# Kernel tuning notes

Measured on AMD Instinct MI355X. Metric: run time of the kernel, lower is better.

Reference implementation:

```python
import jax, jax.numpy as jnp
import numpy as np

B, H, W, C = 32, 56, 56, 384
HEADS, WIN, SHIFT = 12, 7, 3
MLP_HID = 4 * C
N = WIN * WIN
EPS = 1e-5


def _rel_pos_index(win):
    ch, cw = np.meshgrid(np.arange(win), np.arange(win), indexing='ij')
    coords = np.stack([ch.ravel(), cw.ravel()])            # (2, N)
    rel = coords[:, :, None] - coords[:, None, :]          # (2, N, N)
    rel = rel.transpose(1, 2, 0).astype(np.int64)
    rel[:, :, 0] += win - 1
    rel[:, :, 1] += win - 1
    rel[:, :, 0] *= 2 * win - 1
    return rel.sum(-1)                                     # (N, N)


def _attn_mask(Hh, Ww, win, shift):
    img = np.zeros((Hh, Ww))
    cnt = 0
    slices = (slice(0, -win), slice(-win, -shift), slice(-shift, None))
    for hs in slices:
        for ws in slices:
            img[hs, ws] = cnt
            cnt += 1
    m = img.reshape(Hh // win, win, Ww // win, win).transpose(0, 2, 1, 3).reshape(-1, win * win)
    am = m[:, None, :] - m[:, :, None]
    return np.where(am != 0, -100.0, 0.0).astype(np.float32)  # (nW, N, N)


REL_IDX = jnp.asarray(_rel_pos_index(WIN))
ATTN_MASK = jnp.asarray(_attn_mask(H, W, WIN, SHIFT))


def setup_inputs() -> dict:
    key = jax.random.key(0)
    ks = jax.random.split(key, 16)
    s = 0.02
    return {
        'x': jax.random.normal(ks[0], (B, H * W, C), jnp.float32),
        'g1': jnp.ones((C,), jnp.float32),
        'b1': jnp.zeros((C,), jnp.float32),
        'qkv_w': jax.random.normal(ks[1], (3 * C, C), jnp.float32) * s,
        'qkv_b': jnp.zeros((3 * C,), jnp.float32),
        'rel_bias': jax.random.normal(ks[2], ((2 * WIN - 1) ** 2, HEADS), jnp.float32) * s,
        'proj_w': jax.random.normal(ks[3], (C, C), jnp.float32) * s,
        'proj_b': jnp.zeros((C,), jnp.float32),
        'g2': jnp.ones((C,), jnp.float32),
        'b2': jnp.zeros((C,), jnp.float32),
        'fc1_w': jax.random.normal(ks[4], (MLP_HID, C), jnp.float32) * s,
        'fc1_b': jnp.zeros((MLP_HID,), jnp.float32),
        'fc2_w': jax.random.normal(ks[5], (C, MLP_HID), jnp.float32) * s,
        'fc2_b': jnp.zeros((C,), jnp.float32),
    }


def _ln(x, g, b):
    m = x.mean(-1, keepdims=True)
    v = jnp.var(x, axis=-1, keepdims=True)
    return (x - m) * jax.lax.rsqrt(v + EPS) * g + b


def reference(x, g1, b1, qkv_w, qkv_b, rel_bias, proj_w, proj_b, g2, b2, fc1_w, fc1_b, fc2_w, fc2_b):
    Bz, L, Cc = x.shape
    hd = Cc // HEADS
    nWh = H // WIN
    shortcut = x

    h = _ln(x, g1, b1).reshape(Bz, H, W, Cc)
    h = jnp.roll(h, (-SHIFT, -SHIFT), axis=(1, 2))
    # window partition -> (Bz*nW, N, C)
    h = h.reshape(Bz, nWh, WIN, nWh, WIN, Cc).transpose(0, 1, 3, 2, 4, 5).reshape(-1, N, Cc)

    qkv = (h @ qkv_w.T + qkv_b).reshape(-1, N, 3, HEADS, hd).transpose(2, 0, 3, 1, 4)
    q, k, v = qkv[0] * (hd ** -0.5), qkv[1], qkv[2]
    attn = jnp.einsum('bhnd,bhmd->bhnm', q, k)  # (Bz*nW, heads, N, N)

    bias = rel_bias[REL_IDX.reshape(-1)].reshape(N, N, HEADS).transpose(2, 0, 1)
    attn = attn + bias[None]

    nW = ATTN_MASK.shape[0]
    attn = attn.reshape(Bz, nW, HEADS, N, N) + ATTN_MASK[None, :, None]
    attn = jax.nn.softmax(attn, axis=-1).reshape(-1, HEADS, N, N)

    out = jnp.einsum('bhnm,bhmd->bhnd', attn, v).transpose(0, 2, 1, 3).reshape(-1, N, Cc)
    out = out @ proj_w.T + proj_b
    # window reverse + unshift
    out = out.reshape(Bz, nWh, nWh, WIN, WIN, Cc).transpose(0, 1, 3, 2, 4, 5).reshape(Bz, H, W, Cc)
    out = jnp.roll(out, (SHIFT, SHIFT), axis=(1, 2)).reshape(Bz, L, Cc)

    x = shortcut + out
    h2 = _ln(x, g2, b2)
    h2 = jax.nn.gelu(h2 @ fc1_w.T + fc1_b, approximate=False)
    h2 = h2 @ fc2_w.T + fc2_b
    return x + h2
```

## Files before the change

kernel.cpp:

```cpp
#include <hip/hip_runtime.h>
#include <hip/hip_bf16.h>
#include <math.h>

#define B_      32
#define H_      56
#define W_      56
#define C_      384
#define HEADS_  12
#define WIN_    7
#define SHIFT_  3
#define NTOK_   49
#define HD_     32
#define T_      100352
#define MLP_    1536
#define TCH_    50176

typedef __bf16 bf16x8 __attribute__((ext_vector_type(8)));
typedef unsigned short u16x8 __attribute__((ext_vector_type(8)));
typedef float  f32x4  __attribute__((ext_vector_type(4)));

__device__ __forceinline__ float bf2f(unsigned short u) {
  union { unsigned int i; float f; } v; v.i = ((unsigned int)u) << 16; return v.f;
}
__device__ __forceinline__ unsigned short f2bf(float f) {
  union { float f; unsigned int i; } v; v.f = f;
  unsigned int x = v.i;
  return (unsigned short)((x + 0x7fffu + ((x >> 16) & 1u)) >> 16);
}
__device__ __forceinline__ float gelu_fast(float x) {
  const float t = 0.79788456f * x * (1.0f + 0.044715f * x * x);
  const float e = __expf(2.0f * t);
  const float th = 1.0f - 2.0f / (e + 1.0f);
  return 0.5f * x * (1.0f + th);
}
__device__ __forceinline__ void gload_lds16(const void* g, void* l) {
  __builtin_amdgcn_global_load_lds(
      (const __attribute__((address_space(1))) void*)g,
      (__attribute__((address_space(3))) void*)l, 16, 0, 0);
}
__device__ __forceinline__ bf16x8 ldg8(const unsigned short* p) {
  u16x8 v = *(const u16x8*)p;
  return __builtin_bit_cast(bf16x8, v);
}

__global__ __launch_bounds__(256)
void wconv_all_kernel(const float* __restrict__ s0, unsigned short* __restrict__ d0,
                      const float* __restrict__ s1, unsigned short* __restrict__ d1,
                      const float* __restrict__ s2, unsigned short* __restrict__ d2,
                      const float* __restrict__ s3, unsigned short* __restrict__ d3) {
  int b = blockIdx.x;
  const float* src; unsigned short* dst;
  if (b < 432)       { src = s0; dst = d0; }
  else if (b < 576)  { src = s1; dst = d1; b -= 432; }
  else if (b < 1152) { src = s2; dst = d2; b -= 576; }
  else               { src = s3; dst = d3; b -= 1152; }
  const int i = (b * 256 + threadIdx.x) * 4;
  const float4 v = *(const float4*)(src + i);
  ushort4 o;
  o.x = f2bf(v.x); o.y = f2bf(v.y); o.z = f2bf(v.z); o.w = f2bf(v.w);
  *(ushort4*)(dst + i) = o;
}

template<int REMAP>
__global__ __launch_bounds__(256)
void ln_kernel(const float* __restrict__ xin, const float* __restrict__ g,
               const float* __restrict__ bb, unsigned short* __restrict__ outbf) {
  const int m = blockIdx.x * 4 + (threadIdx.x >> 6);
  const int lane = threadIdx.x & 63;
  size_t src;
  if (REMAP) {
    int w = m / NTOK_, t = m - w * NTOK_;
    int bz = w >> 6, widx = w & 63;
    int wh = widx >> 3, ww = widx & 7;
    int ih = t / WIN_, iw = t - ih * WIN_;
    int gh = (wh * WIN_ + ih + SHIFT_) % H_;
    int gw = (ww * WIN_ + iw + SHIFT_) % W_;
    src = ((size_t)bz * (H_ * W_) + gh * W_ + gw) * C_;
  } else {
    src = (size_t)m * C_;
  }
  const float* row = xin + src;
  float v[6]; float s = 0.f, s2 = 0.f;
#pragma unroll
  for (int u = 0; u < 6; ++u) {
    v[u] = row[lane + 64 * u];
    s += v[u]; s2 += v[u] * v[u];
  }
#pragma unroll
  for (int off = 32; off; off >>= 1) {
    s  += __shfl_xor(s, off);
    s2 += __shfl_xor(s2, off);
  }
  const float mean = s * (1.0f / C_);
  const float var  = s2 * (1.0f / C_) - mean * mean;
  const float rstd = rsqrtf(var + 1e-5f);
  unsigned short* orow = outbf + (size_t)m * C_;
#pragma unroll
  for (int u = 0; u < 6; ++u) {
    int c = lane + 64 * u;
    orow[c] = f2bf((v[u] - mean) * rstd * g[c] + bb[c]);
  }
}

#define BM 256
#define BN 128
#define BKg 64

template<int EPI>
__global__ __launch_bounds__(512)
void mfma_gemm(const unsigned short* __restrict__ A,
               const unsigned short* __restrict__ Wb,
               const float* __restrict__ bias,
               void* __restrict__ outv,
               const float* __restrict__ resid,
               int M, int Nn, int K) {
  __shared__ unsigned short Al[BM * BKg];
  __shared__ unsigned short Bl[BN * BKg];
  const int t    = threadIdx.x;
  const int wid  = t >> 6;
  const int lane = t & 63;
  const int wr   = wid >> 1, wc = wid & 1;

  const unsigned int nb = gridDim.x * gridDim.y;
  const unsigned int lin = blockIdx.y * gridDim.x + blockIdx.x;
  const unsigned int q = nb >> 3, r = nb & 7;
  const unsigned int xcd = lin & 7, idx = lin >> 3;
  const unsigned int wg = (xcd < r ? xcd * (q + 1) : r * (q + 1) + (xcd - r) * q) + idx;
  const int m0 = (int)(wg / gridDim.x) * BM;
  const int n0 = (int)(wg % gridDim.x) * BN;

  f32x4 acc[4][4] = {};

  const int sr8    = lane >> 3;
  const int schunk = (lane & 7) ^ (sr8 & 7);
  const int fr  = lane & 15;
  const int fq  = lane >> 4;

  for (int k0 = 0; k0 < K; k0 += BKg) {
    __syncthreads();
#pragma unroll
    for (int i = 0; i < 4; ++i) {
      const int rr = i * 64 + wid * 8 + sr8;
      gload_lds16(A + (size_t)(m0 + rr) * K + k0 + schunk * 8,
                  (void*)(Al + (size_t)(i * 64 + wid * 8) * BKg));
    }
#pragma unroll
    for (int i = 0; i < 2; ++i) {
      const int rr = i * 64 + wid * 8 + sr8;
      gload_lds16(Wb + (size_t)(n0 + rr) * K + k0 + schunk * 8,
                  (void*)(Bl + (size_t)(i * 64 + wid * 8) * BKg));
    }
    __syncthreads();

#pragma unroll
    for (int kk = 0; kk < 2; ++kk) {
      bf16x8 af[4], bfr[4];
#pragma unroll
      for (int mi = 0; mi < 4; ++mi) {
        const int row = wr * 64 + mi * 16 + fr;
        const int ch  = (kk * 4 + fq) ^ (row & 7);
        af[mi] = *(const bf16x8*)(Al + (size_t)row * BKg + ch * 8);
      }
#pragma unroll
      for (int ni = 0; ni < 4; ++ni) {
        const int row = wc * 64 + ni * 16 + fr;
        const int ch  = (kk * 4 + fq) ^ (row & 7);
        bfr[ni] = *(const bf16x8*)(Bl + (size_t)row * BKg + ch * 8);
      }
#pragma unroll
      for (int mi = 0; mi < 4; ++mi)
#pragma unroll
        for (int ni = 0; ni < 4; ++ni)
          acc[mi][ni] = __builtin_amdgcn_mfma_f32_16x16x32_bf16(
              af[mi], bfr[ni], acc[mi][ni], 0, 0, 0);
    }
  }

  const int ecol  = fr;
  const int erow0 = fq * 4;
#pragma unroll
  for (int mi = 0; mi < 4; ++mi) {
#pragma unroll
    for (int r2 = 0; r2 < 4; ++r2) {
      const int m = m0 + wr * 64 + mi * 16 + erow0 + r2;
      size_t dstbase = 0;
      if (EPI == 2) {
        int w = m / NTOK_, tt = m - w * NTOK_;
        int bz = w >> 6, widx = w & 63;
        int wh = widx >> 3, ww = widx & 7;
        int ih = tt / WIN_, iw = tt - ih * WIN_;
        int gh = (wh * WIN_ + ih + SHIFT_) % H_;
        int gw = (ww * WIN_ + iw + SHIFT_) % W_;
        dstbase = ((size_t)bz * (H_ * W_) + gh * W_ + gw) * C_;
      }
#pragma unroll
      for (int ni = 0; ni < 4; ++ni) {
        const int n = n0 + wc * 64 + ni * 16 + ecol;
        float val = acc[mi][ni][r2] + bias[n];
        if (EPI == 0) {
          ((unsigned short*)outv)[(size_t)m * Nn + n] = f2bf(val);
        } else if (EPI == 1) {
          ((unsigned short*)outv)[(size_t)m * Nn + n] = f2bf(gelu_fast(val));
        } else if (EPI == 2) {
          ((float*)outv)[dstbase + n] = resid[dstbase + n] + val;
        } else {
          float* o = (float*)outv + (size_t)m * Nn + n;
          *o += val;
        }
      }
    }
  }
}

__global__ __launch_bounds__(64)
void bias_expand_kernel(const float* __restrict__ rel_bias,
                        float* __restrict__ biasx) {
  const int hi = blockIdx.x;
  const int head = hi / NTOK_, i = hi - head * NTOK_;
  const int j = threadIdx.x;
  float v = 0.f;
  if (j < NTOK_) {
    const int ih = i / 7, iw = i - ih * 7;
    const int jh = j / 7, jw = j - jh * 7;
    const int ridx = (ih - jh + 6) * 13 + (iw - jw + 6);
    v = rel_bias[ridx * HEADS_ + head];
  }
  biasx[(size_t)hi * 64 + j] = v;
}

#define AW 2
__global__ __launch_bounds__(64 * AW)
void attn_mfma_kernel(const unsigned short* __restrict__ qkv,
                      const float* __restrict__ biasx,
                      unsigned short* __restrict__ out) {
  __shared__ unsigned short sP[AW][64 * 72];
  __shared__ unsigned short sVT[AW][32 * 72];
  __shared__ float sRI[AW][64];
  const int wid  = threadIdx.x >> 6;
  const int lane = threadIdx.x & 63;
  const int task = blockIdx.x * AW + wid;
  const int w    = task / HEADS_;
  const int head = task - w * HEADS_;
  const int widx = w & 63;
  const int wh = widx >> 3, ww = widx & 7;
  const bool edge = (wh == 7) || (ww == 7);
  const int c  = lane & 15;
  const int fq = lane >> 4;
  unsigned short* Pl = sP[wid];
  unsigned short* Vl = sVT[wid];
  float* Ri = sRI[wid];
  const unsigned short* qw = qkv + (size_t)w * NTOK_ * (3 * C_);

  u16x8 vv[4];
#pragma unroll
  for (int p = 0; p < 4; ++p)
    vv[p] = *(const u16x8*)(qw + (size_t)(p * 16 + c) * (3 * C_) + 2 * C_ + head * HD_ + fq * 8);

  bf16x8 kf[4], qf[4];
#pragma unroll
  for (int nj = 0; nj < 4; ++nj)
    kf[nj] = ldg8(qw + (size_t)(nj * 16 + c) * (3 * C_) + C_ + head * HD_ + fq * 8);
#pragma unroll
  for (int qi = 0; qi < 4; ++qi)
    qf[qi] = ldg8(qw + (size_t)(qi * 16 + c) * (3 * C_) + head * HD_ + fq * 8);

  const f32x4 zero4 = {0.f, 0.f, 0.f, 0.f};
  f32x4 accT[4][4];
#pragma unroll
  for (int nj = 0; nj < 4; ++nj)
#pragma unroll
    for (int qi = 0; qi < 4; ++qi)
      accT[nj][qi] = __builtin_amdgcn_mfma_f32_16x16x32_bf16(kf[nj], qf[qi], zero4, 0, 0, 0);

#pragma unroll
  for (int p = 0; p < 4; ++p)
#pragma unroll
    for (int u = 0; u < 8; ++u)
      Vl[(fq * 8 + u) * 72 + p * 16 + c] = (unsigned short)vv[p][u];

  int lj16[16];
  unsigned jpad = 0;
#pragma unroll
  for (int tt = 0; tt < 16; ++tt) {
    const int j = (tt >> 2) * 16 + fq * 4 + (tt & 3);
    int lj = 0;
    if (j >= NTOK_) jpad |= (1u << tt);
    else if (edge) {
      const int jh = j / 7, jw2 = j - jh * 7;
      const int shj = wh * 7 + jh, swj = ww * 7 + jw2;
      lj = (shj < 49 ? 0 : (shj < 53 ? 1 : 2)) * 3 + (swj < 49 ? 0 : (swj < 53 ? 1 : 2));
    }
    lj16[tt] = lj;
  }

  const float* bh = biasx + (size_t)head * (NTOK_ * 64);
#pragma unroll
  for (int qi = 0; qi < 4; ++qi) {
    const int i  = qi * 16 + c;
    const int ic = i < NTOK_ ? i : 0;
    int li = 0;
    if (edge) {
      const int ih = ic / 7, iw2 = ic - ih * 7;
      const int shi = wh * 7 + ih, swi = ww * 7 + iw2;
      li = (shi < 49 ? 0 : (shi < 53 ? 1 : 2)) * 3 + (swi < 49 ? 0 : (swi < 53 ? 1 : 2));
    }
    float sv[16];
#pragma unroll
    for (int nj = 0; nj < 4; ++nj) {
      const float4 b4 = *(const float4*)(bh + ic * 64 + nj * 16 + fq * 4);
      const float* b4p = (const float*)&b4;
#pragma unroll
      for (int r = 0; r < 4; ++r) {
        const int tt = nj * 4 + r;
        float s = accT[nj][qi][r] * 0.17677669529663687f + b4p[r];
        if (edge && lj16[tt] != li) s -= 100.f;
        if (jpad & (1u << tt)) s = -1e30f;
        sv[tt] = s;
      }
    }
    float mx = sv[0];
#pragma unroll
    for (int tt = 1; tt < 16; ++tt) mx = fmaxf(mx, sv[tt]);
    mx = fmaxf(mx, __shfl_xor(mx, 16));
    mx = fmaxf(mx, __shfl_xor(mx, 32));
    float e[16]; float sm = 0.f;
#pragma unroll
    for (int tt = 0; tt < 16; ++tt) { e[tt] = __expf(sv[tt] - mx); sm += e[tt]; }
    sm += __shfl_xor(sm, 16);
    sm += __shfl_xor(sm, 32);
    if (fq == 0) Ri[i] = 1.0f / sm;
#pragma unroll
    for (int nj = 0; nj < 4; ++nj) {
      ushort4 pk;
      pk.x = f2bf(e[nj * 4 + 0]); pk.y = f2bf(e[nj * 4 + 1]);
      pk.z = f2bf(e[nj * 4 + 2]); pk.w = f2bf(e[nj * 4 + 3]);
      *(ushort4*)(Pl + (size_t)i * 72 + nj * 16 + fq * 4) = pk;
    }
  }

  f32x4 accO[4][2] = {};
#pragma unroll
  for (int kk = 0; kk < 2; ++kk) {
    bf16x8 ap[4], bv[2];
#pragma unroll
    for (int mi = 0; mi < 4; ++mi)
      ap[mi] = __builtin_bit_cast(bf16x8,
          *(const u16x8*)(Pl + (mi * 16 + c) * 72 + kk * 32 + fq * 8));
#pragma unroll
    for (int nd = 0; nd < 2; ++nd)
      bv[nd] = __builtin_bit_cast(bf16x8,
          *(const u16x8*)(Vl + (nd * 16 + c) * 72 + kk * 32 + fq * 8));
#pragma unroll
    for (int mi = 0; mi < 4; ++mi)
#pragma unroll
      for (int nd = 0; nd < 2; ++nd)
        accO[mi][nd] = __builtin_amdgcn_mfma_f32_16x16x32_bf16(ap[mi], bv[nd], accO[mi][nd], 0, 0, 0);
  }

#pragma unroll
  for (int mi = 0; mi < 4; ++mi)
#pragma unroll
    for (int r = 0; r < 4; ++r) {
      const int i = mi * 16 + fq * 4 + r;
      if (i < NTOK_) {
        const float inv = Ri[i];
#pragma unroll
        for (int nd = 0; nd < 2; ++nd)
          out[(size_t)(w * NTOK_ + i) * C_ + head * HD_ + nd * 16 + c] =
              f2bf(accO[mi][nd][r] * inv);
      }
    }
}

extern "C" void kernel_launch(void* const* d_in, const int* in_sizes, int n_in,
                              void* d_out, int out_size, void* d_ws, size_t ws_size,
                              hipStream_t stream) {
  const float* x        = (const float*)d_in[0];
  const float* g1       = (const float*)d_in[1];
  const float* b1       = (const float*)d_in[2];
  const float* qkv_w    = (const float*)d_in[3];
  const float* qkv_b    = (const float*)d_in[4];
  const float* rel_bias = (const float*)d_in[5];
  const float* proj_w   = (const float*)d_in[6];
  const float* proj_b   = (const float*)d_in[7];
  const float* g2       = (const float*)d_in[8];
  const float* b2       = (const float*)d_in[9];
  const float* fc1_w    = (const float*)d_in[10];
  const float* fc1_b    = (const float*)d_in[11];
  const float* fc2_w    = (const float*)d_in[12];
  const float* fc2_b    = (const float*)d_in[13];
  float* out = (float*)d_out;

  char* ws = (char*)d_ws;
  unsigned short* xw   = (unsigned short*)(ws);
  unsigned short* qkvb = (unsigned short*)(ws + 77070336);
  unsigned short* attn_out = xw;
  unsigned short* h2   = xw;
  unsigned short* hidc = qkvb;
  unsigned short* qkv_wb  = (unsigned short*)(ws + 308412416);
  unsigned short* proj_wb = (unsigned short*)(ws + 309297152);
  unsigned short* fc1_wb  = (unsigned short*)(ws + 309592064);
  unsigned short* fc2_wb  = (unsigned short*)(ws + 310771712);
  float*          biasx   = (float*)(ws + 311951360);

  wconv_all_kernel<<<dim3(1728), dim3(256), 0, stream>>>(
      qkv_w, qkv_wb, proj_w, proj_wb, fc1_w, fc1_wb, fc2_w, fc2_wb);
  bias_expand_kernel<<<dim3(HEADS_ * NTOK_), dim3(64), 0, stream>>>(rel_bias, biasx);

  ln_kernel<1><<<dim3(T_ / 4), dim3(256), 0, stream>>>(x, g1, b1, xw);

  mfma_gemm<0><<<dim3(1152 / BN, T_ / BM), dim3(512), 0, stream>>>(
      xw, qkv_wb, qkv_b, (void*)qkvb, nullptr, T_, 1152, 384);

  attn_mfma_kernel<<<dim3((T_ / NTOK_) * HEADS_ / AW), dim3(64 * AW), 0, stream>>>(
      qkvb, biasx, attn_out);

  mfma_gemm<2><<<dim3(384 / BN, T_ / BM), dim3(512), 0, stream>>>(
      attn_out, proj_wb, proj_b, (void*)out, x, T_, 384, 384);

  ln_kernel<0><<<dim3(T_ / 4), dim3(256), 0, stream>>>(out, g2, b2, h2);

  for (int chk = 0; chk < 2; ++chk) {
    const size_t row0 = (size_t)chk * TCH_;
    mfma_gemm<1><<<dim3(MLP_ / BN, TCH_ / BM), dim3(512), 0, stream>>>(
        h2 + row0 * C_, fc1_wb, fc1_b, (void*)hidc, nullptr, TCH_, MLP_, 384);
    mfma_gemm<3><<<dim3(384 / BN, TCH_ / BM), dim3(512), 0, stream>>>(
        hidc, fc2_wb, fc2_b, (void*)(out + row0 * C_), nullptr, TCH_, 384, MLP_);
  }
}
```

Baseline: 876.1 us.

## Triple-buffer GEMM LDS tiles with split A/B prefetch and explicit vmcnt waits

```diff
diff --git a/kernel.cpp b/kernel.cpp
--- a/kernel.cpp
+++ b/kernel.cpp
@@ -107,15 +107,15 @@
 #define BKg 64
 
 template<int EPI>
-__global__ __launch_bounds__(512)
+__global__ __launch_bounds__(512, 2)
 void mfma_gemm(const unsigned short* __restrict__ A,
                const unsigned short* __restrict__ Wb,
                const float* __restrict__ bias,
                void* __restrict__ outv,
                const float* __restrict__ resid,
                int M, int Nn, int K) {
-  __shared__ unsigned short Al[BM * BKg];
-  __shared__ unsigned short Bl[BN * BKg];
+  __shared__ unsigned short Al[3][BM * BKg];
+  __shared__ unsigned short Bl[3][BN * BKg];
   const int t    = threadIdx.x;
   const int wid  = t >> 6;
   const int lane = t & 63;
@@ -136,45 +136,96 @@
   const int fr  = lane & 15;
   const int fq  = lane >> 4;
 
-  for (int k0 = 0; k0 < K; k0 += BKg) {
-    __syncthreads();
-#pragma unroll
-    for (int i = 0; i < 4; ++i) {
-      const int rr = i * 64 + wid * 8 + sr8;
-      gload_lds16(A + (size_t)(m0 + rr) * K + k0 + schunk * 8,
-                  (void*)(Al + (size_t)(i * 64 + wid * 8) * BKg));
-    }
-#pragma unroll
-    for (int i = 0; i < 2; ++i) {
-      const int rr = i * 64 + wid * 8 + sr8;
-      gload_lds16(Wb + (size_t)(n0 + rr) * K + k0 + schunk * 8,
-                  (void*)(Bl + (size_t)(i * 64 + wid * 8) * BKg));
-    }
-    __syncthreads();
-
-#pragma unroll
-    for (int kk = 0; kk < 2; ++kk) {
+  const int nk = K / BKg;
+
+#define STAGE_A_(kt, b)                                                        \
+  { _Pragma("unroll")                                                          \
+    for (int i = 0; i < 4; ++i) {                                              \
+      const int rr = i * 64 + wid * 8 + sr8;                                   \
+      gload_lds16(A + (size_t)(m0 + rr) * K + (kt) * BKg + schunk * 8,         \
+                  (void*)(&Al[b][(i * 64 + wid * 8) * BKg]));                  \
+    } }
+#define STAGE_B_(kt, b)                                                        \
+  { _Pragma("unroll")                                                          \
+    for (int i = 0; i < 2; ++i) {                                              \
+      const int rr = i * 64 + wid * 8 + sr8;                                   \
+      gload_lds16(Wb + (size_t)(n0 + rr) * K + (kt) * BKg + schunk * 8,        \
+                  (void*)(&Bl[b][(i * 64 + wid * 8) * BKg]));                  \
+    } }
+
+  STAGE_A_(0, 0); STAGE_B_(0, 0);
+  STAGE_A_(1, 1); STAGE_B_(1, 1);
+
+  for (int u = 0; u < nk; ++u) {
+    const int cur = u % 3;
+    const int stg = (u + 2) % 3;
+    const unsigned short* Ab = &Al[cur][0];
+    const unsigned short* Bb = &Bl[cur][0];
+
+    if (u + 2 < nk) { STAGE_A_(u + 2, stg); }
+    if (u + 2 < nk)      { asm volatile("s_waitcnt vmcnt(10)" ::: "memory"); }
+    else if (u + 1 < nk) { asm volatile("s_waitcnt vmcnt(6)"  ::: "memory"); }
+    else                 { asm volatile("s_waitcnt vmcnt(0)"  ::: "memory"); }
+    __builtin_amdgcn_sched_barrier(0);
+    __builtin_amdgcn_s_barrier();
+    __builtin_amdgcn_sched_barrier(0);
+    {
       bf16x8 af[4], bfr[4];
 #pragma unroll
       for (int mi = 0; mi < 4; ++mi) {
         const int row = wr * 64 + mi * 16 + fr;
-        const int ch  = (kk * 4 + fq) ^ (row & 7);
-        af[mi] = *(const bf16x8*)(Al + (size_t)row * BKg + ch * 8);
+        const int ch  = fq ^ (row & 7);
+        af[mi] = *(const bf16x8*)(Ab + (size_t)row * BKg + ch * 8);
       }
 #pragma unroll
       for (int ni = 0; ni < 4; ++ni) {
         const int row = wc * 64 + ni * 16 + fr;
-        const int ch  = (kk * 4 + fq) ^ (row & 7);
-        bfr[ni] = *(const bf16x8*)(Bl + (size_t)row * BKg + ch * 8);
-      }
+        const int ch  = fq ^ (row & 7);
+        bfr[ni] = *(const bf16x8*)(Bb + (size_t)row * BKg + ch * 8);
+      }
+      __builtin_amdgcn_s_setprio(1);
 #pragma unroll
       for (int mi = 0; mi < 4; ++mi)
 #pragma unroll
         for (int ni = 0; ni < 4; ++ni)
           acc[mi][ni] = __builtin_amdgcn_mfma_f32_16x16x32_bf16(
               af[mi], bfr[ni], acc[mi][ni], 0, 0, 0);
-    }
-  }
+      __builtin_amdgcn_s_setprio(0);
+    }
+    __builtin_amdgcn_sched_barrier(0);
+    __builtin_amdgcn_s_barrier();
+    __builtin_amdgcn_sched_barrier(0);
+
+    if (u + 2 < nk) { STAGE_B_(u + 2, stg); }
+    {
+      bf16x8 af[4], bfr[4];
+#pragma unroll
+      for (int mi = 0; mi < 4; ++mi) {
+        const int row = wr * 64 + mi * 16 + fr;
+        const int ch  = (4 + fq) ^ (row & 7);
+        af[mi] = *(const bf16x8*)(Ab + (size_t)row * BKg + ch * 8);
+      }
+#pragma unroll
+      for (int ni = 0; ni < 4; ++ni) {
+        const int row = wc * 64 + ni * 16 + fr;
+        const int ch  = (4 + fq) ^ (row & 7);
+        bfr[ni] = *(const bf16x8*)(Bb + (size_t)row * BKg + ch * 8);
+      }
+      __builtin_amdgcn_s_setprio(1);
+#pragma unroll
+      for (int mi = 0; mi < 4; ++mi)
+#pragma unroll
+        for (int ni = 0; ni < 4; ++ni)
+          acc[mi][ni] = __builtin_amdgcn_mfma_f32_16x16x32_bf16(
+              af[mi], bfr[ni], acc[mi][ni], 0, 0, 0);
+      __builtin_amdgcn_s_setprio(0);
+    }
+    __builtin_amdgcn_sched_barrier(0);
+    __builtin_amdgcn_s_barrier();
+    __builtin_amdgcn_sched_barrier(0);
+  }
+#undef STAGE_A_
+#undef STAGE_B_
 
   const int ecol  = fr;
   const int erow0 = fq * 4;
```

Measured after the change: 1.111 ms. 1.27x slower.
